# Kernel optimization log

Hardware: AMD Instinct MI355X
Metric: run time of the kernel (lower is better)

## Reference

```python
import jax, jax.numpy as jnp
import numpy as np

NUM_HEADS = 16
NUM_LANDMARKS = 64
N_ITER = 6


def iterative_inv(mat):
    # mat: (B, H, L, L) row-stochastic kernel; Newton-Schulz-style iteration
    L = mat.shape[-1]
    I = jnp.eye(L, dtype=mat.dtype)
    K = mat
    # init: V = K^T / max_j(sum_i K_ij)
    denom = jnp.max(jnp.sum(K, axis=-2), axis=-1)[:, :, None, None]
    Vm = (1.0 / denom) * jnp.swapaxes(K, -1, -2)
    for _ in range(N_ITER):
        KV = jnp.matmul(K, Vm)
        Vm = jnp.matmul(0.25 * Vm, 13.0 * I - jnp.matmul(KV, 15.0 * I - jnp.matmul(KV, 7.0 * I - KV)))
    return Vm


def setup_inputs() -> dict:
    key = jax.random.key(0)
    kq, kk, kv = jax.random.split(key, 3)
    B, N, C = 4, 4096, 1024
    return {
        "Q": jax.random.normal(kq, (B, N, C), dtype=jnp.float32),
        "K": jax.random.normal(kk, (B, N, C), dtype=jnp.float32),
        "V": jax.random.normal(kv, (B, N, C), dtype=jnp.float32),
    }


def reference(Q, K, V):
    B, N, C = Q.shape
    H, Lm = NUM_HEADS, NUM_LANDMARKS
    hd = C // H
    scale = hd ** 0.5
    # (B, H, N, hd)
    q = Q.reshape(B, N, H, hd).transpose(0, 2, 1, 3) / scale
    k = K.reshape(B, N, H, hd).transpose(0, 2, 1, 3)
    v = V.reshape(B, N, H, hd).transpose(0, 2, 1, 3)

    # landmark pooling (N divisible by Lm): mean over segments of length N//Lm
    seg = N // Lm
    k_lm = k.reshape(B, H, Lm, seg, hd).mean(axis=-2)  # (B,H,Lm,hd)
    q_lm = q.reshape(B, H, Lm, seg, hd).mean(axis=-2)  # (B,H,Lm,hd)

    kernel_1 = jax.nn.softmax(jnp.einsum('bhnd,bhld->bhnl', q, k_lm), axis=-1)   # (B,H,N,Lm)
    kernel_2 = jax.nn.softmax(jnp.einsum('bhmd,bhld->bhml', q_lm, k_lm), axis=-1)  # (B,H,Lm,Lm)
    kernel_3 = jax.nn.softmax(jnp.einsum('bhld,bhnd->bhln', q_lm, k), axis=-1)   # (B,H,Lm,N)

    out = jnp.matmul(jnp.matmul(kernel_1, iterative_inv(kernel_2)), jnp.matmul(kernel_3, v))
    return out.transpose(0, 2, 1, 3).reshape(B, N, C)
```

## Files before the change

### kernel.cpp

```cpp
#include <hip/hip_runtime.h>
#include <math.h>

#define BB 4
#define NN 4096
#define CC 1024
#define HH 16
#define HD 64
#define LM 64
#define SEG 64
#define BHN (BB*HH)
#define MATP 68
#define MATE (64*MATP)
#define NTILE 32
#define APROW 4160

typedef __attribute__((ext_vector_type(8))) short bf16x8;
typedef __attribute__((ext_vector_type(4))) short s16x4;
typedef __attribute__((ext_vector_type(4))) float f32x4;

__device__ __forceinline__ float shfl_sum16(float v) {
  v += __shfl_xor(v, 1, 16);
  v += __shfl_xor(v, 2, 16);
  v += __shfl_xor(v, 4, 16);
  v += __shfl_xor(v, 8, 16);
  return v;
}

__device__ __forceinline__ void split8(const float* f, bf16x8& hi, bf16x8& lo) {
#pragma unroll
  for (int i = 0; i < 8; ++i) {
    unsigned u = __builtin_bit_cast(unsigned, f[i]);
    float hf = __builtin_bit_cast(float, u & 0xFFFF0000u);
    hi[i] = (short)(u >> 16);
    float l = f[i] - hf;
    unsigned ul = __builtin_bit_cast(unsigned, l);
    lo[i] = (short)(ul >> 16);
  }
}

__device__ __forceinline__ void split4(const float* f, s16x4& hi, s16x4& lo) {
#pragma unroll
  for (int i = 0; i < 4; ++i) {
    unsigned u = __builtin_bit_cast(unsigned, f[i]);
    float hf = __builtin_bit_cast(float, u & 0xFFFF0000u);
    hi[i] = (short)(u >> 16);
    float l = f[i] - hf;
    unsigned ul = __builtin_bit_cast(unsigned, l);
    lo[i] = (short)(ul >> 16);
  }
}

__device__ __forceinline__ int planeAddr(int row, int cd) {
  int B = (row << 7) + (cd << 4);
  return B ^ ((row & 7) << 4);
}
__device__ __forceinline__ bf16x8 ldP(const short* __restrict__ P, int row, int cd) {
  return *(const bf16x8*)((const char*)P + planeAddr(row, cd));
}

__device__ __forceinline__ void xpose4(float x[4], int lane) {
  bool p1 = (lane >> 4) & 1;
  float s0 = p1 ? x[0] : x[1], s1 = p1 ? x[2] : x[3];
  float r0 = __shfl_xor(s0, 16, 64), r1 = __shfl_xor(s1, 16, 64);
  if (p1) { x[0] = r0; x[2] = r1; } else { x[1] = r0; x[3] = r1; }
  bool p2 = (lane >> 5) & 1;
  s0 = p2 ? x[0] : x[2]; s1 = p2 ? x[1] : x[3];
  r0 = __shfl_xor(s0, 32, 64); r1 = __shfl_xor(s1, 32, 64);
  if (p2) { x[0] = r0; x[1] = r1; } else { x[2] = r0; x[3] = r1; }
}

__global__ __launch_bounds__(256) void lm_kernel(
    const float* __restrict__ Q, const float* __restrict__ K,
    float* __restrict__ qlm, float* __restrict__ klm) {
  int bh = blockIdx.y; int b = bh >> 4; int h = bh & 15;
  int tid = threadIdx.x;
  int l = blockIdx.x * 4 + (tid >> 6);
  int d = tid & 63;
  const float* qbase = Q + ((size_t)b*NN + (size_t)l*SEG)*CC + h*HD + d;
  const float* kbase = K + ((size_t)b*NN + (size_t)l*SEG)*CC + h*HD + d;
  float sq = 0.f, sk = 0.f;
#pragma unroll 8
  for (int s = 0; s < SEG; ++s) {
    sq += qbase[(size_t)s*CC];
    sk += kbase[(size_t)s*CC];
  }
  qlm[(size_t)bh*4096 + l*64 + d] = sq * (1.0f/(64.0f*8.0f));
  klm[(size_t)bh*4096 + l*64 + d] = sk * (1.0f/64.0f);
}

__global__ __launch_bounds__(256, 3) void k3v_kernel(
    const float* __restrict__ K, const float* __restrict__ V,
    const float* __restrict__ qlm, float* __restrict__ ACC3p) {
  __shared__ alignas(16) short KEh[64*64], KEl[64*64];
  __shared__ alignas(16) short VtH[64*64], VtL[64*64];
  __shared__ alignas(16) float Erow[64*MATP];
  const int bh = blockIdx.y, b = bh >> 4, h = bh & 15;
  const int tile = blockIdx.x, tid = threadIdx.x;
  const int wid = tid >> 6, lane = tid & 63;
  const int lr = lane & 15, lg = lane >> 4;
  const int m0 = wid*16 + lg*4;

  bf16x8 qh[2], ql[2];
#pragma unroll
  for (int ks = 0; ks < 2; ++ks) {
    const float* qp = qlm + (size_t)bh*4096 + (wid*16 + lr)*64 + ks*32 + lg*8;
    float qf[8];
    *(float4*)&qf[0] = *(const float4*)qp;
    *(float4*)&qf[4] = *(const float4*)(qp + 4);
    split8(qf, qh[ks], ql[ks]);
  }

  f32x4 acc2[4];
#pragma unroll
  for (int t = 0; t < 4; ++t) acc2[t] = (f32x4){0.f, 0.f, 0.f, 0.f};
  float srow[4] = {0.f, 0.f, 0.f, 0.f};

  const int rk0 = tid >> 3,        ck = tid & 7;
  const int rk1 = (tid + 256) >> 3;
  const int dV  = 4*lr + lg;

  float4 gk[2][2], gv[4];

#define K3V_LOAD(SUB)                                                          \
  {                                                                            \
    const int n0_ = tile*128 + (SUB)*64;                                       \
    const float* kb0 = &K[((size_t)b*NN + n0_ + rk0)*CC + h*HD + ck*8];        \
    const float* kb1 = &K[((size_t)b*NN + n0_ + rk1)*CC + h*HD + ck*8];        \
    gk[0][0] = *(const float4*)kb0;  gk[0][1] = *(const float4*)(kb0 + 4);     \
    gk[1][0] = *(const float4*)kb1;  gk[1][1] = *(const float4*)(kb1 + 4);     \
    _Pragma("unroll")                                                          \
    for (int q = 0; q < 4; ++q) {                                              \
      int f = tid + 256*q;                                                     \
      int r = f >> 4, c4 = (f & 15) << 2;                                      \
      gv[q] = *(const float4*)&V[((size_t)b*NN + n0_ + r)*CC + h*HD + c4];     \
    }                                                                          \
  }

#define K3V_WRITE()                                                            \
  {                                                                            \
    _Pragma("unroll")                                                          \
    for (int q2 = 0; q2 < 2; ++q2) {                                           \
      float kf[8];                                                             \
      *(float4*)&kf[0] = gk[q2][0];                                            \
      *(float4*)&kf[4] = gk[q2][1];                                            \
      bf16x8 khv, klv; split8(kf, khv, klv);                                   \
      int r = q2 ? rk1 : rk0;                                                  \
      int A = planeAddr(r, ck);                                                \
      *(bf16x8*)((char*)KEh + A) = khv;                                        \
      *(bf16x8*)((char*)KEl + A) = klv;                                        \
    }                                                                          \
    _Pragma("unroll")                                                          \
    for (int q = 0; q < 4; ++q) {                                              \
      float x[4] = {gv[q].x, gv[q].y, gv[q].z, gv[q].w};                       \
      xpose4(x, lane);                                                         \
      int nb = 16*q + 4*wid;                                                   \
      s16x4 vh, vl; split4(x, vh, vl);                                         \
      int B = (dV << 7) + (nb << 1);                                           \
      B ^= (dV & 7) << 4;                                                      \
      *(s16x4*)((char*)VtH + B) = vh;                                          \
      *(s16x4*)((char*)VtL + B) = vl;                                          \
    }                                                                          \
  }

#define K3V_COMPUTE()                                                          \
  {                                                                            \
    f32x4 zacc[4];                                                             \
    _Pragma("unroll")                                                          \
    for (int t = 0; t < 4; ++t) zacc[t] = (f32x4){0.f, 0.f, 0.f, 0.f};        \
    _Pragma("unroll")                                                          \
    for (int ks = 0; ks < 2; ++ks) {                                           \
      _Pragma("unroll")                                                        \
      for (int tn = 0; tn < 4; ++tn) {                                         \
        bf16x8 bh_ = ldP(KEh, tn*16 + lr, 4*ks + lg);                          \
        bf16x8 bl_ = ldP(KEl, tn*16 + lr, 4*ks + lg);                          \
        zacc[tn] = __builtin_amdgcn_mfma_f32_16x16x32_bf16(qh[ks], bh_, zacc[tn], 0, 0, 0); \
        zacc[tn] = __builtin_amdgcn_mfma_f32_16x16x32_bf16(qh[ks], bl_, zacc[tn], 0, 0, 0); \
        zacc[tn] = __builtin_amdgcn_mfma_f32_16x16x32_bf16(ql[ks], bh_, zacc[tn], 0, 0, 0); \
      }                                                                        \
    }                                                                          \
    float e[4][4];                                                             \
    _Pragma("unroll")                                                          \
    for (int tn = 0; tn < 4; ++tn)                                             \
      _Pragma("unroll")                                                        \
      for (int r = 0; r < 4; ++r) e[tn][r] = __expf(zacc[tn][r]);              \
    _Pragma("unroll")                                                          \
    for (int r = 0; r < 4; ++r) {                                              \
      float t = e[0][r] + e[1][r] + e[2][r] + e[3][r];                         \
      srow[r] += shfl_sum16(t);                                                \
    }                                                                          \
    _Pragma("unroll")                                                          \
    for (int tn = 0; tn < 4; ++tn) {                                           \
      const int n = tn*16 + lr;                                                \
      _Pragma("unroll")                                                        \
      for (int r = 0; r < 4; ++r) Erow[(m0 + r)*MATP + n] = e[tn][r];          \
    }                                                                          \
    _Pragma("unroll")                                                          \
    for (int ks = 0; ks < 2; ++ks) {                                           \
      float fa[8];                                                             \
      const float* ap = Erow + (wid*16 + lr)*MATP + ks*32 + lg*8;              \
      *(float4*)&fa[0] = *(const float4*)ap;                                   \
      *(float4*)&fa[4] = *(const float4*)(ap + 4);                             \
      bf16x8 ah, al; split8(fa, ah, al);                                       \
      _Pragma("unroll")                                                        \
      for (int tn = 0; tn < 4; ++tn) {                                         \
        bf16x8 bh_ = ldP(VtH, tn*16 + lr, 4*ks + lg);                          \
        bf16x8 bl_ = ldP(VtL, tn*16 + lr, 4*ks + lg);                          \
        acc2[tn] = __builtin_amdgcn_mfma_f32_16x16x32_bf16(ah, bh_, acc2[tn], 0, 0, 0); \
        acc2[tn] = __builtin_amdgcn_mfma_f32_16x16x32_bf16(ah, bl_, acc2[tn], 0, 0, 0); \
        acc2[tn] = __builtin_amdgcn_mfma_f32_16x16x32_bf16(al, bh_, acc2[tn], 0, 0, 0); \
      }                                                                        \
    }                                                                          \
  }

  K3V_LOAD(0)
  K3V_WRITE()
  __syncthreads();
  K3V_LOAD(1)
  K3V_COMPUTE()
  __syncthreads();
  K3V_WRITE()
  __syncthreads();
  K3V_COMPUTE()

  float* accp = ACC3p + ((size_t)tile*BHN + bh)*APROW;
  if (lr == 0) {
#pragma unroll
    for (int r = 0; r < 4; ++r) accp[4096 + m0 + r] = srow[r];
  }
#pragma unroll
  for (int tn = 0; tn < 4; ++tn)
#pragma unroll
    for (int r = 0; r < 4; ++r)
      accp[(m0 + r)*64 + tn*16 + lr] = acc2[tn][r];
}

__global__ __launch_bounds__(256) void reduce_kernel(
    const float* __restrict__ ACC3p, float* __restrict__ ACC3, float* __restrict__ S3) {
  const int bh = blockIdx.y;
  const int f4 = blockIdx.x*256 + threadIdx.x;
  if (f4 >= APROW/4) return;
  float4 s = make_float4(0.f, 0.f, 0.f, 0.f);
  const float* base = ACC3p + (size_t)bh*APROW + f4*4;
#pragma unroll 4
  for (int t = 0; t < NTILE; ++t) {
    float4 v = *(const float4*)(base + (size_t)t*BHN*APROW);
    s.x += v.x; s.y += v.y; s.z += v.z; s.w += v.w;
  }
  const int f = f4*4;
  if (f < 4096) *(float4*)&ACC3[(size_t)bh*4096 + f] = s;
  else          *(float4*)&S3[bh*64 + (f - 4096)] = s;
}

template<bool FUSE, bool HR, bool HC, bool HG>
__device__ __forceinline__ void mm_mfma(
    const float* __restrict__ Arow, const float* __restrict__ Scol,
    float diagc, float scale,
    float* __restrict__ OutRow, float* __restrict__ OutCol, float* __restrict__ OutGlob,
    int wr, int tn, int lane) {
  const int lr = lane & 15, lg = lane >> 4;
  f32x4 acc = (f32x4){0.f, 0.f, 0.f, 0.f};

#pragma unroll
  for (int ks = 0; ks < 2; ++ks) {
    const int kb = ks*32 + lg*8;
    float fa[8];
    const float* ap = Arow + (wr*16 + lr)*MATP + kb;
    *(float4*)&fa[0] = *(const float4*)ap;
    *(float4*)&fa[4] = *(const float4*)(ap + 4);
    bf16x8 ah, al; split8(fa, ah, al);
    float fb[8];
    const float* bp = Scol + (tn*16 + lr)*MATP + kb;
    *(float4*)&fb[0] = *(const float4*)bp;
    *(float4*)&fb[4] = *(const float4*)(bp + 4);
    if (FUSE) {
      int diff = (tn*16 + lr) - kb;
#pragma unroll
      for (int i = 0; i < 8; ++i) fb[i] = (i == diff ? diagc : 0.f) - fb[i];
    }
    bf16x8 bh_, bl_; split8(fb, bh_, bl_);
    acc = __builtin_amdgcn_mfma_f32_16x16x32_bf16(ah, bh_, acc, 0, 0, 0);
    acc = __builtin_amdgcn_mfma_f32_16x16x32_bf16(ah, bl_, acc, 0, 0, 0);
    acc = __builtin_amdgcn_mfma_f32_16x16x32_bf16(al, bh_, acc, 0, 0, 0);
  }
  __syncthreads();
  const int n = tn*16 + lr, m0 = wr*16 + lg*4;
  float v0 = scale*acc[0], v1 = scale*acc[1], v2 = scale*acc[2], v3 = scale*acc[3];
  if (HC) *(float4*)&OutCol[n*MATP + m0] = make_float4(v0, v1, v2, v3);
  if (HR) {
    OutRow[(m0+0)*MATP + n] = v0;
    OutRow[(m0+1)*MATP + n] = v1;
    OutRow[(m0+2)*MATP + n] = v2;
    OutRow[(m0+3)*MATP + n] = v3;
  }
  if (HG) {
    OutGlob[(m0+0)*64 + n] = v0;
    OutGlob[(m0+1)*64 + n] = v1;
    OutGlob[(m0+2)*64 + n] = v2;
    OutGlob[(m0+3)*64 + n] = v3;
  }
  __syncthreads();
}

__global__ __launch_bounds__(1024, 1) void inv_kernel(
    const float* __restrict__ qlm, const float* __restrict__ klm,
    const float* __restrict__ S3, const float* __restrict__ ACC3,
    float* __restrict__ W) {
  extern __shared__ float sm[];
  float* K2row = sm;
  float* Vmrow = sm + 1*MATE;
  float* Vmcol = sm + 2*MATE;
  float* Xrow  = sm + 3*MATE;
  float* Xcol  = sm + 4*MATE;
  float* Ycol  = sm + 5*MATE;
  float* Zcol  = sm + 6*MATE;
  float* rs    = sm + 7*MATE;
  float* rinv  = rs + 256;
  float* red   = rinv + 64;
  const int bh = blockIdx.x, tid = threadIdx.x;
  const int wid = tid >> 6, lane = tid & 63;
  const int wr = wid & 3, tn = wid >> 2;
  const int lr = lane & 15, lg = lane >> 4;
  const int m0 = wr*16 + lg*4, n = tn*16 + lr;

  {
    int f = tid, r = f >> 4, c4 = (f & 15) << 2;
    *(float4*)&Xrow[r*MATP + c4] = *(const float4*)&qlm[(size_t)bh*4096 + f*4];
    *(float4*)&Xcol[r*MATP + c4] = *(const float4*)&klm[(size_t)bh*4096 + f*4];
  }
  __syncthreads();

  {
    f32x4 zacc = (f32x4){0.f, 0.f, 0.f, 0.f};
#pragma unroll
    for (int ks = 0; ks < 2; ++ks) {
      const int kb = ks*32 + lg*8;
      float fa[8];
      const float* ap = Xrow + (wr*16 + lr)*MATP + kb;
      *(float4*)&fa[0] = *(const float4*)ap;
      *(float4*)&fa[4] = *(const float4*)(ap + 4);
      bf16x8 ah, al; split8(fa, ah, al);
      float fb[8];
      const float* bp = Xcol + (tn*16 + lr)*MATP + kb;
      *(float4*)&fb[0] = *(const float4*)bp;
      *(float4*)&fb[4] = *(const float4*)(bp + 4);
      bf16x8 bh_, bl_; split8(fb, bh_, bl_);
      zacc = __builtin_amdgcn_mfma_f32_16x16x32_bf16(ah, bh_, zacc, 0, 0, 0);
      zacc = __builtin_amdgcn_mfma_f32_16x16x32_bf16(ah, bl_, zacc, 0, 0, 0);
      zacc = __builtin_amdgcn_mfma_f32_16x16x32_bf16(al, bh_, zacc, 0, 0, 0);
    }
    float e[4];
#pragma unroll
    for (int r = 0; r < 4; ++r) e[r] = __expf(zacc[r]);
    float part[4];
#pragma unroll
    for (int r = 0; r < 4; ++r) part[r] = shfl_sum16(e[r]);
    if (lr == 0) {
#pragma unroll
      for (int r = 0; r < 4; ++r) rs[(m0 + r)*4 + tn] = part[r];
    }
    __syncthreads();
    if (tid < 64)
      rinv[tid] = 1.0f / (rs[tid*4] + rs[tid*4+1] + rs[tid*4+2] + rs[tid*4+3]);
    __syncthreads();
#pragma unroll
    for (int r = 0; r < 4; ++r)
      K2row[(m0+r)*MATP + n] = e[r] * rinv[m0 + r];
  }
  __syncthreads();

  if (tid < 64) {
    float c = 0.f;
#pragma unroll 8
    for (int i = 0; i < 64; ++i) c += K2row[i*MATP + tid];
#pragma unroll
    for (int m = 1; m < 64; m <<= 1) c = fmaxf(c, __shfl_xor(c, m, 64));
    if (tid == 0) red[0] = 1.0f / c;
  }
  __syncthreads();
  const float invden = red[0];

  {
    int f = tid, i = f >> 4, c4 = (f & 15) << 2;
    float4 kv = *(const float4*)&K2row[i*MATP + c4];
    kv.x *= invden; kv.y *= invden; kv.z *= invden; kv.w *= invden;
    *(float4*)&Vmcol[i*MATP + c4] = kv;
    Vmrow[(c4+0)*MATP + i] = kv.x;
    Vmrow[(c4+1)*MATP + i] = kv.y;
    Vmrow[(c4+2)*MATP + i] = kv.z;
    Vmrow[(c4+3)*MATP + i] = kv.w;
  }
  __syncthreads();

  for (int it = 0; it < 6; ++it) {
    mm_mfma<false, true,  true,  false>(K2row, Vmcol, 0.f,  1.0f,  Xrow, Xcol, nullptr, wr, tn, lane);
    mm_mfma<true,  false, true,  false>(Xrow,  Xcol,  7.f,  1.0f,  nullptr, Ycol, nullptr, wr, tn, lane);
    mm_mfma<true,  false, true,  false>(Xrow,  Ycol,  15.f, 1.0f,  nullptr, Zcol, nullptr, wr, tn, lane);
    mm_mfma<true,  true,  true,  false>(Vmrow, Zcol,  13.f, 0.25f, Vmrow, Vmcol, nullptr, wr, tn, lane);
  }

  {
    int f = tid, k = f >> 4, c4 = (f & 15) << 2;
    float4 tv = *(const float4*)&ACC3[(size_t)bh*4096 + f*4];
    float ri = 1.0f / S3[bh*64 + k];
    Ycol[(c4+0)*MATP + k] = tv.x * ri;
    Ycol[(c4+1)*MATP + k] = tv.y * ri;
    Ycol[(c4+2)*MATP + k] = tv.z * ri;
    Ycol[(c4+3)*MATP + k] = tv.w * ri;
  }
  __syncthreads();
  mm_mfma<false, false, false, true>(Vmrow, Ycol, 0.f, 1.0f, nullptr, nullptr, W + (size_t)bh*4096, wr, tn, lane);
}

__global__ __launch_bounds__(256, 4) void out_kernel(
    const float* __restrict__ Q, const float* __restrict__ klm,
    const float* __restrict__ W, float* __restrict__ Out) {
  __shared__ alignas(16) short WtH[64*64], WtL[64*64];
  __shared__ alignas(16) float Prow[64*MATP];
  const int bh = blockIdx.y, b = bh >> 4, h = bh & 15;
  const int n0 = blockIdx.x * 64;
  const int tid = threadIdx.x;
  const int wid = tid >> 6, lane = tid & 63;
  const int lr = lane & 15, lg = lane >> 4;
  const int m0 = wid*16 + lg*4;

  const int dW = 4*lr + lg;
#pragma unroll
  for (int q = 0; q < 4; ++q) {
    int f = tid + 256*q;
    int r = f >> 4, c4 = (f & 15) << 2;
    float4 wv = *(const float4*)&W[(size_t)bh*4096 + r*64 + c4];
    float x[4] = {wv.x, wv.y, wv.z, wv.w};
    xpose4(x, lane);
    int nb = 16*q + 4*wid;
    s16x4 wh, wl; split4(x, wh, wl);
    int B = (dW << 7) + (nb << 1);
    B ^= (dW & 7) << 4;
    *(s16x4*)((char*)WtH + B) = wh;
    *(s16x4*)((char*)WtL + B) = wl;
  }

  bf16x8 qh[2], qlo[2];
#pragma unroll
  for (int ks = 0; ks < 2; ++ks) {
    const float* qp = Q + ((size_t)b*NN + n0 + wid*16 + lr)*CC + h*HD + ks*32 + lg*8;
    float qf[8];
    *(float4*)&qf[0] = *(const float4*)qp;
    *(float4*)&qf[4] = *(const float4*)(qp + 4);
#pragma unroll
    for (int i = 0; i < 8; ++i) qf[i] *= 0.125f;
    split8(qf, qh[ks], qlo[ks]);
  }

  f32x4 zacc[4];
#pragma unroll
  for (int t = 0; t < 4; ++t) zacc[t] = (f32x4){0.f, 0.f, 0.f, 0.f};
#pragma unroll
  for (int tn = 0; tn < 4; ++tn) {
    const float* kp = &klm[(size_t)bh*4096 + (tn*16 + lr)*64 + lg*8];
    float4 k00 = *(const float4*)kp;
    float4 k01 = *(const float4*)(kp + 4);
    float4 k10 = *(const float4*)(kp + 32);
    float4 k11 = *(const float4*)(kp + 36);
    float kf[8];
    *(float4*)&kf[0] = k00; *(float4*)&kf[4] = k01;
    bf16x8 b0h, b0l; split8(kf, b0h, b0l);
    *(float4*)&kf[0] = k10; *(float4*)&kf[4] = k11;
    bf16x8 b1h, b1l; split8(kf, b1h, b1l);
    zacc[tn] = __builtin_amdgcn_mfma_f32_16x16x32_bf16(qh[0], b0h, zacc[tn], 0, 0, 0);
    zacc[tn] = __builtin_amdgcn_mfma_f32_16x16x32_bf16(qh[0], b0l, zacc[tn], 0, 0, 0);
    zacc[tn] = __builtin_amdgcn_mfma_f32_16x16x32_bf16(qlo[0], b0h, zacc[tn], 0, 0, 0);
    zacc[tn] = __builtin_amdgcn_mfma_f32_16x16x32_bf16(qh[1], b1h, zacc[tn], 0, 0, 0);
    zacc[tn] = __builtin_amdgcn_mfma_f32_16x16x32_bf16(qh[1], b1l, zacc[tn], 0, 0, 0);
    zacc[tn] = __builtin_amdgcn_mfma_f32_16x16x32_bf16(qlo[1], b1h, zacc[tn], 0, 0, 0);
  }
  float e[4][4];
#pragma unroll
  for (int tn = 0; tn < 4; ++tn)
#pragma unroll
    for (int r = 0; r < 4; ++r) e[tn][r] = __expf(zacc[tn][r]);
#pragma unroll
  for (int r = 0; r < 4; ++r) {
    float t = e[0][r] + e[1][r] + e[2][r] + e[3][r];
    t = shfl_sum16(t);
    float ri = 1.0f / t;
#pragma unroll
    for (int tn = 0; tn < 4; ++tn) e[tn][r] *= ri;
  }
#pragma unroll
  for (int tn = 0; tn < 4; ++tn) {
    const int n = tn*16 + lr;
#pragma unroll
    for (int r = 0; r < 4; ++r) Prow[(m0+r)*MATP + n] = e[tn][r];
  }
  __syncthreads();

  f32x4 oacc[4];
#pragma unroll
  for (int t = 0; t < 4; ++t) oacc[t] = (f32x4){0.f, 0.f, 0.f, 0.f};
#pragma unroll
  for (int ks = 0; ks < 2; ++ks) {
    float fa[8];
    const float* ap = Prow + (wid*16 + lr)*MATP + ks*32 + lg*8;
    *(float4*)&fa[0] = *(const float4*)ap;
    *(float4*)&fa[4] = *(const float4*)(ap + 4);
    bf16x8 ah, al; split8(fa, ah, al);
#pragma unroll
    for (int tn = 0; tn < 4; ++tn) {
      bf16x8 bh_ = ldP(WtH, tn*16 + lr, 4*ks + lg);
      bf16x8 bl_ = ldP(WtL, tn*16 + lr, 4*ks + lg);
      oacc[tn] = __builtin_amdgcn_mfma_f32_16x16x32_bf16(ah, bh_, oacc[tn], 0, 0, 0);
      oacc[tn] = __builtin_amdgcn_mfma_f32_16x16x32_bf16(ah, bl_, oacc[tn], 0, 0, 0);
      oacc[tn] = __builtin_amdgcn_mfma_f32_16x16x32_bf16(al, bh_, oacc[tn], 0, 0, 0);
    }
  }
#pragma unroll
  for (int tn = 0; tn < 4; ++tn) {
    const int d = tn*16 + lr;
#pragma unroll
    for (int r = 0; r < 4; ++r)
      Out[((size_t)b*NN + n0 + m0 + r)*CC + h*HD + d] = oacc[tn][r];
  }
}

extern "C" void kernel_launch(void* const* d_in, const int* in_sizes, int n_in,
                              void* d_out, int out_size, void* d_ws, size_t ws_size,
                              hipStream_t stream) {
  const float* Q = (const float*)d_in[0];
  const float* K = (const float*)d_in[1];
  const float* V = (const float*)d_in[2];
  float* out = (float*)d_out;
  float* ws  = (float*)d_ws;

  float* qlm   = ws;
  float* klm   = ws + 262144;
  float* S3    = ws + 524288;
  float* ACC3  = ws + 528384;
  float* Wm    = ws + 790528;
  float* ACC3p = ws + 1052672;

  size_t shC = (size_t)(7*MATE + 384)*sizeof(float);
  hipFuncSetAttribute((const void*)inv_kernel,
                      hipFuncAttributeMaxDynamicSharedMemorySize, (int)shC);

  lm_kernel    <<<dim3(16, BHN), 256, 0, stream>>>(Q, K, qlm, klm);
  k3v_kernel   <<<dim3(NTILE, BHN), 256, 0, stream>>>(K, V, qlm, ACC3p);
  reduce_kernel<<<dim3(5, BHN), 256, 0, stream>>>(ACC3p, ACC3, S3);
  inv_kernel   <<<dim3(BHN),    1024, shC, stream>>>(qlm, klm, S3, ACC3, Wm);
  out_kernel   <<<dim3(64, BHN), 256, 0, stream>>>(Q, klm, Wm, out);
}
```

Before: 150.5 us.

## Restructure k3v kernel to split N across waves and keep softmax weights in registers

The k3v kernel changes how work is split across its four waves. Each wave now takes 16 of the n positions for all 64 landmarks, instead of 16 landmarks for all n, and computes the transposed product with the Q-landmark fragments held in registers. The exp weights are packed into bf16 hi/lo pairs and redistributed by lane shuffles straight into MFMA operands, so the fp32 Erow shared-memory round trip goes away. The price is a cross-wave reduction of the partial outputs through shared memory at the end, half-empty MFMA B operands (lanes with lg>=2 feed zeros), and per-wave row-sum partials that enlarge APROW and add work to the reduce kernel.

```diff
diff --git a/kernel.cpp b/kernel.cpp
--- a/kernel.cpp
+++ b/kernel.cpp
@@ -12,11 +12,12 @@
 #define MATP 68
 #define MATE (64*MATP)
 #define NTILE 32
-#define APROW 4160
+#define APROW 4352
 
 typedef __attribute__((ext_vector_type(8))) short bf16x8;
 typedef __attribute__((ext_vector_type(4))) short s16x4;
 typedef __attribute__((ext_vector_type(4))) float f32x4;
+typedef __attribute__((ext_vector_type(4))) unsigned u32x4;
 
 __device__ __forceinline__ float shfl_sum16(float v) {
   v += __shfl_xor(v, 1, 16);
@@ -48,6 +49,27 @@
     unsigned ul = __builtin_bit_cast(unsigned, l);
     lo[i] = (short)(ul >> 16);
   }
+}
+
+__device__ __forceinline__ void packsplit4(const float e[4],
+    unsigned& h01, unsigned& h23, unsigned& l01, unsigned& l23) {
+  unsigned u0 = __builtin_bit_cast(unsigned, e[0]);
+  unsigned u1 = __builtin_bit_cast(unsigned, e[1]);
+  unsigned u2 = __builtin_bit_cast(unsigned, e[2]);
+  unsigned u3 = __builtin_bit_cast(unsigned, e[3]);
+  h01 = (u0 >> 16) | (u1 & 0xFFFF0000u);
+  h23 = (u2 >> 16) | (u3 & 0xFFFF0000u);
+  float r0 = e[0] - __builtin_bit_cast(float, u0 & 0xFFFF0000u);
+  float r1 = e[1] - __builtin_bit_cast(float, u1 & 0xFFFF0000u);
+  float r2 = e[2] - __builtin_bit_cast(float, u2 & 0xFFFF0000u);
+  float r3 = e[3] - __builtin_bit_cast(float, u3 & 0xFFFF0000u);
+  l01 = (__builtin_bit_cast(unsigned, r0) >> 16) | (__builtin_bit_cast(unsigned, r1) & 0xFFFF0000u);
+  l23 = (__builtin_bit_cast(unsigned, r2) >> 16) | (__builtin_bit_cast(unsigned, r3) & 0xFFFF0000u);
+}
+
+__device__ __forceinline__ bf16x8 mk8(unsigned w0, unsigned w1, unsigned w2, unsigned w3) {
+  u32x4 u = (u32x4){w0, w1, w2, w3};
+  return __builtin_bit_cast(bf16x8, u);
 }
 
 __device__ __forceinline__ int planeAddr(int row, int cd) {
@@ -91,34 +113,38 @@
 __global__ __launch_bounds__(256, 3) void k3v_kernel(
     const float* __restrict__ K, const float* __restrict__ V,
     const float* __restrict__ qlm, float* __restrict__ ACC3p) {
-  __shared__ alignas(16) short KEh[64*64], KEl[64*64];
-  __shared__ alignas(16) short VtH[64*64], VtL[64*64];
-  __shared__ alignas(16) float Erow[64*MATP];
+  __shared__ alignas(16) char SM[32768];
+  short* KEh = (short*)SM;
+  short* KEl = (short*)(SM + 8192);
+  short* VtH = (short*)(SM + 16384);
+  short* VtL = (short*)(SM + 24576);
   const int bh = blockIdx.y, b = bh >> 4, h = bh & 15;
   const int tile = blockIdx.x, tid = threadIdx.x;
   const int wid = tid >> 6, lane = tid & 63;
   const int lr = lane & 15, lg = lane >> 4;
-  const int m0 = wid*16 + lg*4;
-
-  bf16x8 qh[2], ql[2];
-#pragma unroll
-  for (int ks = 0; ks < 2; ++ks) {
-    const float* qp = qlm + (size_t)bh*4096 + (wid*16 + lr)*64 + ks*32 + lg*8;
-    float qf[8];
-    *(float4*)&qf[0] = *(const float4*)qp;
-    *(float4*)&qf[4] = *(const float4*)(qp + 4);
-    split8(qf, qh[ks], ql[ks]);
-  }
-
-  f32x4 acc2[4];
-#pragma unroll
-  for (int t = 0; t < 4; ++t) acc2[t] = (f32x4){0.f, 0.f, 0.f, 0.f};
-  float srow[4] = {0.f, 0.f, 0.f, 0.f};
-
-  const int rk0 = tid >> 3,        ck = tid & 7;
+  const int dV = 4*lr + lg;
+
+  bf16x8 qbh[4][2], qbl[4][2];
+#pragma unroll
+  for (int lt = 0; lt < 4; ++lt)
+#pragma unroll
+    for (int ks = 0; ks < 2; ++ks) {
+      const float* qp = qlm + (size_t)bh*4096 + (lt*16 + lr)*64 + ks*32 + lg*8;
+      float qf[8];
+      *(float4*)&qf[0] = *(const float4*)qp;
+      *(float4*)&qf[4] = *(const float4*)(qp + 4);
+      split8(qf, qbh[lt][ks], qbl[lt][ks]);
+    }
+
+  f32x4 acc2[4][4];
+#pragma unroll
+  for (int i = 0; i < 4; ++i)
+#pragma unroll
+    for (int j = 0; j < 4; ++j) acc2[i][j] = (f32x4){0.f, 0.f, 0.f, 0.f};
+  float srw[4] = {0.f, 0.f, 0.f, 0.f};
+
+  const int rk0 = tid >> 3, ck = tid & 7;
   const int rk1 = (tid + 256) >> 3;
-  const int dV  = 4*lr + lg;
-
   float4 gk[2][2], gv[4];
 
 #define K3V_LOAD(SUB)                                                          \
@@ -164,50 +190,63 @@
 
 #define K3V_COMPUTE()                                                          \
   {                                                                            \
+                                      \
     f32x4 zacc[4];                                                             \
     _Pragma("unroll")                                                          \
     for (int t = 0; t < 4; ++t) zacc[t] = (f32x4){0.f, 0.f, 0.f, 0.f};        \
     _Pragma("unroll")                                                          \
     for (int ks = 0; ks < 2; ++ks) {                                           \
+      bf16x8 kh_ = ldP(KEh, wid*16 + lr, 4*ks + lg);                           \
+      bf16x8 kl_ = ldP(KEl, wid*16 + lr, 4*ks + lg);                           \
       _Pragma("unroll")                                                        \
-      for (int tn = 0; tn < 4; ++tn) {                                         \
-        bf16x8 bh_ = ldP(KEh, tn*16 + lr, 4*ks + lg);                          \
-        bf16x8 bl_ = ldP(KEl, tn*16 + lr, 4*ks + lg);                          \
-        zacc[tn] = __builtin_amdgcn_mfma_f32_16x16x32_bf16(qh[ks], bh_, zacc[tn], 0, 0, 0); \
-        zacc[tn] = __builtin_amdgcn_mfma_f32_16x16x32_bf16(qh[ks], bl_, zacc[tn], 0, 0, 0); \
-        zacc[tn] = __builtin_amdgcn_mfma_f32_16x16x32_bf16(ql[ks], bh_, zacc[tn], 0, 0, 0); \
+      for (int lt = 0; lt < 4; ++lt) {                                         \
+        zacc[lt] = __builtin_amdgcn_mfma_f32_16x16x32_bf16(kh_, qbh[lt][ks], zacc[lt], 0, 0, 0); \
+        zacc[lt] = __builtin_amdgcn_mfma_f32_16x16x32_bf16(kh_, qbl[lt][ks], zacc[lt], 0, 0, 0); \
+        zacc[lt] = __builtin_amdgcn_mfma_f32_16x16x32_bf16(kl_, qbh[lt][ks], zacc[lt], 0, 0, 0); \
       }                                                                        \
     }                                                                          \
-    float e[4][4];                                                             \
-    _Pragma("unroll")                                                          \
-    for (int tn = 0; tn < 4; ++tn)                                             \
+                      \
+    unsigned h01[4], h23[4], l01[4], l23[4];                                   \
+    _Pragma("unroll")                                                          \
+    for (int lt = 0; lt < 4; ++lt) {                                           \
+      float e[4];                                                              \
       _Pragma("unroll")                                                        \
-      for (int r = 0; r < 4; ++r) e[tn][r] = __expf(zacc[tn][r]);              \
-    _Pragma("unroll")                                                          \
-    for (int r = 0; r < 4; ++r) {                                              \
-      float t = e[0][r] + e[1][r] + e[2][r] + e[3][r];                         \
-      srow[r] += shfl_sum16(t);                                                \
+      for (int r = 0; r < 4; ++r) e[r] = __expf(zacc[lt][r]);                  \
+      float s = e[0] + e[1] + e[2] + e[3];                                     \
+      s += __shfl_xor(s, 16, 64);                                              \
+      s += __shfl_xor(s, 32, 64);                                              \
+      srw[lt] += s;                                                            \
+      packsplit4(e, h01[lt], h23[lt], l01[lt], l23[lt]);                       \
     }                                                                          \
-    _Pragma("unroll")                                                          \
-    for (int tn = 0; tn < 4; ++tn) {                                           \
-      const int n = tn*16 + lr;                                                \
+     \
+    const int src0 = (lr + ((2*lg) << 4)) & 63;                                \
+    const int src1 = (lr + ((2*lg + 1) << 4)) & 63;                            \
+    const bool act = (lg < 2);                                                 \
+    bf16x8 Bh[4], Bl[4];                                                       \
+    _Pragma("unroll")                                                          \
+    for (int lt = 0; lt < 4; ++lt) {                                           \
+      unsigned a0 = __shfl(h01[lt], src0, 64), a1 = __shfl(h23[lt], src0, 64); \
+      unsigned a2 = __shfl(h01[lt], src1, 64), a3 = __shfl(h23[lt], src1, 64); \
+      unsigned c0 = __shfl(l01[lt], src0, 64), c1 = __shfl(l23[lt], src0, 64); \
+      unsigned c2 = __shfl(l01[lt], src1, 64), c3 = __shfl(l23[lt], src1, 64); \
+      Bh[lt] = act ? mk8(a0, a1, a2, a3) : mk8(0, 0, 0, 0);                    \
+      Bl[lt] = act ? mk8(c0, c1, c2, c3) : mk8(0, 0, 0, 0);                    \
+    }                                                                          \
+    _Pragma("unroll")                                                          \
+    for (int dt = 0; dt < 4; ++dt) {                                           \
+      bf16x8 vh = mk8(0,0,0,0), vl = mk8(0,0,0,0);                             \
+      if (act) {                                                               \
+        int d_ = dt*16 + lr;                                                   \
+        int off = (d_ << 7) + ((wid*16 + lg*8) << 1);                          \
+        off ^= (d_ & 7) << 4;                                                  \
+        vh = *(const bf16x8*)((const char*)VtH + off);                         \
+        vl = *(const bf16x8*)((const char*)VtL + off);                         \
+      }                                                                        \
       _Pragma("unroll")                                                        \
-      for (int r = 0; r < 4; ++r) Erow[(m0 + r)*MATP + n] = e[tn][r];          \
-    }                                                                          \
-    _Pragma("unroll")                                                          \
-    for (int ks = 0; ks < 2; ++ks) {                                           \
-      float fa[8];                                                             \
-      const float* ap = Erow + (wid*16 + lr)*MATP + ks*32 + lg*8;              \
-      *(float4*)&fa[0] = *(const float4*)ap;                                   \
-      *(float4*)&fa[4] = *(const float4*)(ap + 4);                             \
-      bf16x8 ah, al; split8(fa, ah, al);                                       \
-      _Pragma("unroll")                                                        \
-      for (int tn = 0; tn < 4; ++tn) {                                         \
-        bf16x8 bh_ = ldP(VtH, tn*16 + lr, 4*ks + lg);                          \
-        bf16x8 bl_ = ldP(VtL, tn*16 + lr, 4*ks + lg);                          \
-        acc2[tn] = __builtin_amdgcn_mfma_f32_16x16x32_bf16(ah, bh_, acc2[tn], 0, 0, 0); \
-        acc2[tn] = __builtin_amdgcn_mfma_f32_16x16x32_bf16(ah, bl_, acc2[tn], 0, 0, 0); \
-        acc2[tn] = __builtin_amdgcn_mfma_f32_16x16x32_bf16(al, bh_, acc2[tn], 0, 0, 0); \
+      for (int lt = 0; lt < 4; ++lt) {                                         \
+        acc2[dt][lt] = __builtin_amdgcn_mfma_f32_16x16x32_bf16(vh, Bh[lt], acc2[dt][lt], 0, 0, 0); \
+        acc2[dt][lt] = __builtin_amdgcn_mfma_f32_16x16x32_bf16(vh, Bl[lt], acc2[dt][lt], 0, 0, 0); \
+        acc2[dt][lt] = __builtin_amdgcn_mfma_f32_16x16x32_bf16(vl, Bh[lt], acc2[dt][lt], 0, 0, 0); \
       }                                                                        \
     }                                                                          \
   }
@@ -222,33 +261,83 @@
   __syncthreads();
   K3V_COMPUTE()
 
+  __syncthreads();
+  float4* slotA = (float4*)SM;
+  float4* slotB = (float4*)(SM + 16384);
+  if (wid == 1 || wid == 3) {
+    float4* s = (wid == 1) ? slotA : slotB;
+#pragma unroll
+    for (int dt = 0; dt < 4; ++dt)
+#pragma unroll
+      for (int lt = 0; lt < 4; ++lt)
+        s[(dt*4 + lt)*64 + lane] = make_float4(acc2[dt][lt][0], acc2[dt][lt][1], acc2[dt][lt][2], acc2[dt][lt][3]);
+  }
+  __syncthreads();
+  if (wid == 0 || wid == 2) {
+    float4* s = (wid == 0) ? slotA : slotB;
+#pragma unroll
+    for (int dt = 0; dt < 4; ++dt)
+#pragma unroll
+      for (int lt = 0; lt < 4; ++lt) {
+        float4 v = s[(dt*4 + lt)*64 + lane];
+        acc2[dt][lt][0] += v.x; acc2[dt][lt][1] += v.y; acc2[dt][lt][2] += v.z; acc2[dt][lt][3] += v.w;
+      }
+  }
+  __syncthreads();
+  if (wid == 2) {
+#pragma unroll
+    for (int dt = 0; dt < 4; ++dt)
+#pragma unroll
+      for (int lt = 0; lt < 4; ++lt)
+        slotA[(dt*4 + lt)*64 + lane] = make_float4(acc2[dt][lt][0], acc2[dt][lt][1], acc2[dt][lt][2], acc2[dt][lt][3]);
+  }
+  __syncthreads();
   float* accp = ACC3p + ((size_t)tile*BHN + bh)*APROW;
-  if (lr == 0) {
-#pragma unroll
-    for (int r = 0; r < 4; ++r) accp[4096 + m0 + r] = srow[r];
-  }
-#pragma unroll
-  for (int tn = 0; tn < 4; ++tn)
-#pragma unroll
-    for (int r = 0; r < 4; ++r)
-      accp[(m0 + r)*64 + tn*16 + lr] = acc2[tn][r];
+  if (wid == 0) {
+#pragma unroll
+    for (int dt = 0; dt < 4; ++dt)
+#pragma unroll
+      for (int lt = 0; lt < 4; ++lt) {
+        float4 v = slotA[(dt*4 + lt)*64 + lane];
+        acc2[dt][lt][0] += v.x; acc2[dt][lt][1] += v.y; acc2[dt][lt][2] += v.z; acc2[dt][lt][3] += v.w;
+        *(float4*)&accp[(lt*16 + lr)*64 + dt*16 + lg*4] =
+            make_float4(acc2[dt][lt][0], acc2[dt][lt][1], acc2[dt][lt][2], acc2[dt][lt][3]);
+      }
+  }
+  if (lg == 0) {
+#pragma unroll
+    for (int lt = 0; lt < 4; ++lt)
+      accp[4096 + wid*64 + lt*16 + lr] = srw[lt];
+  }
 }
 
 __global__ __launch_bounds__(256) void reduce_kernel(
     const float* __restrict__ ACC3p, float* __restrict__ ACC3, float* __restrict__ S3) {
   const int bh = blockIdx.y;
   const int f4 = blockIdx.x*256 + threadIdx.x;
-  if (f4 >= APROW/4) return;
-  float4 s = make_float4(0.f, 0.f, 0.f, 0.f);
-  const float* base = ACC3p + (size_t)bh*APROW + f4*4;
+  if (f4 < 1024) {
+    float4 s = make_float4(0.f, 0.f, 0.f, 0.f);
+    const float* base = ACC3p + (size_t)bh*APROW + f4*4;
 #pragma unroll 4
-  for (int t = 0; t < NTILE; ++t) {
-    float4 v = *(const float4*)(base + (size_t)t*BHN*APROW);
-    s.x += v.x; s.y += v.y; s.z += v.z; s.w += v.w;
-  }
-  const int f = f4*4;
-  if (f < 4096) *(float4*)&ACC3[(size_t)bh*4096 + f] = s;
-  else          *(float4*)&S3[bh*64 + (f - 4096)] = s;
+    for (int t = 0; t < NTILE; ++t) {
+      float4 v = *(const float4*)(base + (size_t)t*BHN*APROW);
+      s.x += v.x; s.y += v.y; s.z += v.z; s.w += v.w;
+    }
+    *(float4*)&ACC3[(size_t)bh*4096 + f4*4] = s;
+  } else if (f4 < 1040) {
+    const int l0 = (f4 - 1024)*4;
+    float4 s = make_float4(0.f, 0.f, 0.f, 0.f);
+    const float* base = ACC3p + (size_t)bh*APROW + 4096 + l0;
+    for (int t = 0; t < NTILE; ++t) {
+      const float* tb = base + (size_t)t*BHN*APROW;
+#pragma unroll
+      for (int w = 0; w < 4; ++w) {
+        float4 v = *(const float4*)(tb + w*64);
+        s.x += v.x; s.y += v.y; s.z += v.z; s.w += v.w;
+      }
+    }
+    *(float4*)&S3[bh*64 + l0] = s;
+  }
 }
 
 template<bool FUSE, bool HR, bool HC, bool HG>
```

Result: slower. 192.0 us (+27.6%).

## Fuse K landmark pooling into k3v and replace partial-sum reduce with atomics

Applied to the files above, without the earlier changes.

Moves the K landmark mean into the k3v kernel, which already streams K, so K is read from HBM only once. The separate partial-buffer reduction kernel is removed; per-tile partial results are accumulated directly into ACC3 and S3 with float atomicAdd after a memset. Shared memory is shrunk by reusing the K plane as the exp staging buffer, and occupancy is raised to 4 blocks per SM. The cost is atomic contention of 32 tiles on each element, nondeterministic summation order, and extra syncs.

```diff
diff --git a/kernel.cpp b/kernel.cpp
--- a/kernel.cpp
+++ b/kernel.cpp
@@ -12,7 +12,6 @@
 #define MATP 68
 #define MATE (64*MATP)
 #define NTILE 32
-#define APROW 4160
 
 typedef __attribute__((ext_vector_type(8))) short bf16x8;
 typedef __attribute__((ext_vector_type(4))) short s16x4;
@@ -69,36 +68,36 @@
   if (p2) { x[0] = r0; x[1] = r1; } else { x[2] = r0; x[3] = r1; }
 }
 
-__global__ __launch_bounds__(256) void lm_kernel(
-    const float* __restrict__ Q, const float* __restrict__ K,
-    float* __restrict__ qlm, float* __restrict__ klm) {
+__global__ __launch_bounds__(256) void lm_q_kernel(
+    const float* __restrict__ Q, float* __restrict__ qlm) {
   int bh = blockIdx.y; int b = bh >> 4; int h = bh & 15;
   int tid = threadIdx.x;
   int l = blockIdx.x * 4 + (tid >> 6);
   int d = tid & 63;
   const float* qbase = Q + ((size_t)b*NN + (size_t)l*SEG)*CC + h*HD + d;
-  const float* kbase = K + ((size_t)b*NN + (size_t)l*SEG)*CC + h*HD + d;
-  float sq = 0.f, sk = 0.f;
+  float sq = 0.f;
 #pragma unroll 8
-  for (int s = 0; s < SEG; ++s) {
-    sq += qbase[(size_t)s*CC];
-    sk += kbase[(size_t)s*CC];
-  }
+  for (int s = 0; s < SEG; ++s) sq += qbase[(size_t)s*CC];
   qlm[(size_t)bh*4096 + l*64 + d] = sq * (1.0f/(64.0f*8.0f));
-  klm[(size_t)bh*4096 + l*64 + d] = sk * (1.0f/64.0f);
-}
-
-__global__ __launch_bounds__(256, 3) void k3v_kernel(
+}
+
+__global__ __launch_bounds__(256, 4) void k3v_kernel(
     const float* __restrict__ K, const float* __restrict__ V,
-    const float* __restrict__ qlm, float* __restrict__ ACC3p) {
-  __shared__ alignas(16) short KEh[64*64], KEl[64*64];
-  __shared__ alignas(16) short VtH[64*64], VtL[64*64];
-  __shared__ alignas(16) float Erow[64*MATP];
+    const float* __restrict__ qlm, float* __restrict__ klm,
+    float* __restrict__ S3, float* __restrict__ ACC3) {
+  __shared__ alignas(16) char PlaneA[16384];
+  __shared__ alignas(16) char PlaneB[16384];
+  __shared__ alignas(16) float kred[256];
+  short* KEh = (short*)PlaneA;
+  short* KEl = (short*)(PlaneA + 8192);
+  short* VtH = (short*)PlaneB;
+  short* VtL = (short*)(PlaneB + 8192);
   const int bh = blockIdx.y, b = bh >> 4, h = bh & 15;
   const int tile = blockIdx.x, tid = threadIdx.x;
   const int wid = tid >> 6, lane = tid & 63;
   const int lr = lane & 15, lg = lane >> 4;
   const int m0 = wid*16 + lg*4;
+  const int dV = 4*lr + lg;
 
   bf16x8 qh[2], ql[2];
 #pragma unroll
@@ -114,11 +113,10 @@
 #pragma unroll
   for (int t = 0; t < 4; ++t) acc2[t] = (f32x4){0.f, 0.f, 0.f, 0.f};
   float srow[4] = {0.f, 0.f, 0.f, 0.f};
-
-  const int rk0 = tid >> 3,        ck = tid & 7;
+  float ee[4][4];
+
+  const int rk0 = tid >> 3, ck = tid & 7;
   const int rk1 = (tid + 256) >> 3;
-  const int dV  = 4*lr + lg;
-
   float4 gk[2][2], gv[4];
 
 #define K3V_LOAD(SUB)                                                          \
@@ -149,6 +147,23 @@
       *(bf16x8*)((char*)KEh + A) = khv;                                        \
       *(bf16x8*)((char*)KEl + A) = klv;                                        \
     }                                                                          \
+               \
+    {                                                                          \
+      float s8[8];                                                             \
+      s8[0] = gk[0][0].x + gk[1][0].x;  s8[1] = gk[0][0].y + gk[1][0].y;       \
+      s8[2] = gk[0][0].z + gk[1][0].z;  s8[3] = gk[0][0].w + gk[1][0].w;       \
+      s8[4] = gk[0][1].x + gk[1][1].x;  s8[5] = gk[0][1].y + gk[1][1].y;       \
+      s8[6] = gk[0][1].z + gk[1][1].z;  s8[7] = gk[0][1].w + gk[1][1].w;       \
+      _Pragma("unroll")                                                        \
+      for (int m = 8; m < 64; m <<= 1) {                                       \
+        _Pragma("unroll")                                                      \
+        for (int i = 0; i < 8; ++i) s8[i] += __shfl_xor(s8[i], m, 64);         \
+      }                                                                        \
+      if (lane < 8) {                                                          \
+        *(float4*)&kred[wid*64 + lane*8]     = make_float4(s8[0], s8[1], s8[2], s8[3]); \
+        *(float4*)&kred[wid*64 + lane*8 + 4] = make_float4(s8[4], s8[5], s8[6], s8[7]); \
+      }                                                                        \
+    }                                                                          \
     _Pragma("unroll")                                                          \
     for (int q = 0; q < 4; ++q) {                                              \
       float x[4] = {gv[q].x, gv[q].y, gv[q].z, gv[q].w};                       \
@@ -162,7 +177,13 @@
     }                                                                          \
   }
 
-#define K3V_COMPUTE()                                                          \
+#define K3V_KFIN(SUB)                                                          \
+  if (tid < 64) {                                                              \
+    klm[(size_t)bh*4096 + (tile*2 + (SUB))*64 + tid] =                         \
+        (kred[tid] + kred[64+tid] + kred[128+tid] + kred[192+tid]) * (1.0f/64.0f); \
+  }
+
+#define K3V_GEMM1()                                                            \
   {                                                                            \
     f32x4 zacc[4];                                                             \
     _Pragma("unroll")                                                          \
@@ -178,28 +199,37 @@
         zacc[tn] = __builtin_amdgcn_mfma_f32_16x16x32_bf16(ql[ks], bh_, zacc[tn], 0, 0, 0); \
       }                                                                        \
     }                                                                          \
-    float e[4][4];                                                             \
     _Pragma("unroll")                                                          \
     for (int tn = 0; tn < 4; ++tn)                                             \
       _Pragma("unroll")                                                        \
-      for (int r = 0; r < 4; ++r) e[tn][r] = __expf(zacc[tn][r]);              \
+      for (int r = 0; r < 4; ++r) ee[tn][r] = __expf(zacc[tn][r]);             \
     _Pragma("unroll")                                                          \
     for (int r = 0; r < 4; ++r) {                                              \
-      float t = e[0][r] + e[1][r] + e[2][r] + e[3][r];                         \
+      float t = ee[0][r] + ee[1][r] + ee[2][r] + ee[3][r];                     \
       srow[r] += shfl_sum16(t);                                                \
     }                                                                          \
+  }
+
+#define K3V_EG2()                                                              \
+  {                                                                            \
     _Pragma("unroll")                                                          \
     for (int tn = 0; tn < 4; ++tn) {                                           \
-      const int n = tn*16 + lr;                                                \
       _Pragma("unroll")                                                        \
-      for (int r = 0; r < 4; ++r) Erow[(m0 + r)*MATP + n] = e[tn][r];          \
+      for (int r = 0; r < 4; ++r) {                                            \
+        int row = m0 + r;                                                      \
+        int byte = row*256 + (tn*16 + lr)*4;                                   \
+        byte ^= (row & 7) << 4;                                                \
+        *(float*)(PlaneA + byte) = ee[tn][r];                                  \
+      }                                                                        \
     }                                                                          \
     _Pragma("unroll")                                                          \
     for (int ks = 0; ks < 2; ++ks) {                                           \
+      int row = wid*16 + lr;                                                   \
+      int swz = (row & 7) << 4;                                                \
+      int base = row*256 + ks*128 + lg*32;                                     \
       float fa[8];                                                             \
-      const float* ap = Erow + (wid*16 + lr)*MATP + ks*32 + lg*8;              \
-      *(float4*)&fa[0] = *(const float4*)ap;                                   \
-      *(float4*)&fa[4] = *(const float4*)(ap + 4);                             \
+      *(float4*)&fa[0] = *(const float4*)(PlaneA + (base ^ swz));              \
+      *(float4*)&fa[4] = *(const float4*)(PlaneA + ((base + 16) ^ swz));       \
       bf16x8 ah, al; split8(fa, ah, al);                                       \
       _Pragma("unroll")                                                        \
       for (int tn = 0; tn < 4; ++tn) {                                         \
@@ -216,39 +246,28 @@
   K3V_WRITE()
   __syncthreads();
   K3V_LOAD(1)
-  K3V_COMPUTE()
+  K3V_GEMM1()
+  K3V_KFIN(0)
+  __syncthreads();
+  K3V_EG2()
   __syncthreads();
   K3V_WRITE()
   __syncthreads();
-  K3V_COMPUTE()
-
-  float* accp = ACC3p + ((size_t)tile*BHN + bh)*APROW;
+  K3V_GEMM1()
+  K3V_KFIN(1)
+  __syncthreads();
+  K3V_EG2()
+
   if (lr == 0) {
 #pragma unroll
-    for (int r = 0; r < 4; ++r) accp[4096 + m0 + r] = srow[r];
+    for (int r = 0; r < 4; ++r)
+      atomicAdd(&S3[bh*64 + m0 + r], srow[r]);
   }
 #pragma unroll
   for (int tn = 0; tn < 4; ++tn)
 #pragma unroll
     for (int r = 0; r < 4; ++r)
-      accp[(m0 + r)*64 + tn*16 + lr] = acc2[tn][r];
-}
-
-__global__ __launch_bounds__(256) void reduce_kernel(
-    const float* __restrict__ ACC3p, float* __restrict__ ACC3, float* __restrict__ S3) {
-  const int bh = blockIdx.y;
-  const int f4 = blockIdx.x*256 + threadIdx.x;
-  if (f4 >= APROW/4) return;
-  float4 s = make_float4(0.f, 0.f, 0.f, 0.f);
-  const float* base = ACC3p + (size_t)bh*APROW + f4*4;
-#pragma unroll 4
-  for (int t = 0; t < NTILE; ++t) {
-    float4 v = *(const float4*)(base + (size_t)t*BHN*APROW);
-    s.x += v.x; s.y += v.y; s.z += v.z; s.w += v.w;
-  }
-  const int f = f4*4;
-  if (f < 4096) *(float4*)&ACC3[(size_t)bh*4096 + f] = s;
-  else          *(float4*)&S3[bh*64 + (f - 4096)] = s;
+      atomicAdd(&ACC3[(size_t)bh*4096 + (m0 + r)*64 + tn*16 + lr], acc2[tn][r]);
 }
 
 template<bool FUSE, bool HR, bool HC, bool HG>
@@ -531,20 +550,20 @@
   float* out = (float*)d_out;
   float* ws  = (float*)d_ws;
 
-  float* qlm   = ws;
-  float* klm   = ws + 262144;
-  float* S3    = ws + 524288;
-  float* ACC3  = ws + 528384;
-  float* Wm    = ws + 790528;
-  float* ACC3p = ws + 1052672;
+  float* qlm  = ws;
+  float* klm  = ws + 262144;
+  float* S3   = ws + 524288;
+  float* ACC3 = ws + 528384;
+  float* Wm   = ws + 790528;
 
   size_t shC = (size_t)(7*MATE + 384)*sizeof(float);
   hipFuncSetAttribute((const void*)inv_kernel,
                       hipFuncAttributeMaxDynamicSharedMemorySize, (int)shC);
 
-  lm_kernel    <<<dim3(16, BHN), 256, 0, stream>>>(Q, K, qlm, klm);
-  k3v_kernel   <<<dim3(NTILE, BHN), 256, 0, stream>>>(K, V, qlm, ACC3p);
-  reduce_kernel<<<dim3(5, BHN), 256, 0, stream>>>(ACC3p, ACC3, S3);
-  inv_kernel   <<<dim3(BHN),    1024, shC, stream>>>(qlm, klm, S3, ACC3, Wm);
-  out_kernel   <<<dim3(64, BHN), 256, 0, stream>>>(Q, klm, Wm, out);
-}
+  hipMemsetAsync(S3, 0, (4096 + 262144)*sizeof(float), stream);
+
+  lm_q_kernel<<<dim3(16, BHN), 256, 0, stream>>>(Q, qlm);
+  k3v_kernel <<<dim3(NTILE, BHN), 256, 0, stream>>>(K, V, qlm, klm, S3, ACC3);
+  inv_kernel <<<dim3(BHN),    1024, shC, stream>>>(qlm, klm, S3, ACC3, Wm);
+  out_kernel <<<dim3(64, BHN), 256, 0, stream>>>(Q, klm, Wm, out);
+}
```

New measurement: 154.2 us. 1.02x slower.
